# Optimization experiments

Hardware: AMD Instinct MI355X
Metric: run time of the kernel (lower is better)

## Reference

```python
import jax, jax.numpy as jnp
import numpy as np

N = 100000
E = 800000
DROPOUT_P = 0.5


def setup_inputs() -> dict:
    key = jax.random.key(0)
    ks = jax.random.split(key, 5)
    x = jax.random.normal(ks[0], (N, 128), dtype=jnp.float32)
    edge_index = jax.random.randint(ks[1], (2, E), 0, N, dtype=jnp.int32)
    # Glorot-ish init for the two GCNConv weight matrices
    W1 = jax.random.normal(ks[2], (128, 512), dtype=jnp.float32) * (1.0 / np.sqrt(128))
    b1 = jnp.zeros((512,), dtype=jnp.float32)
    W2 = jax.random.normal(ks[3], (512, 40), dtype=jnp.float32) * (1.0 / np.sqrt(512))
    b2 = jnp.zeros((40,), dtype=jnp.float32)
    return {"x": x, "edge_index": edge_index, "W1": W1, "b1": b1, "W2": W2, "b2": b2}


def _gcn_norm(edge_index, num_nodes):
    # PyG GCNConv: add self-loops, symmetric normalization D^{-1/2} (A+I) D^{-1/2}
    loop = jnp.arange(num_nodes, dtype=edge_index.dtype)
    src = jnp.concatenate([edge_index[0], loop])
    dst = jnp.concatenate([edge_index[1], loop])
    deg = jax.ops.segment_sum(jnp.ones_like(dst, dtype=jnp.float32), dst,
                              num_segments=num_nodes)
    deg_inv_sqrt = jax.lax.rsqrt(deg)  # deg >= 1 thanks to self-loops
    norm = deg_inv_sqrt[src] * deg_inv_sqrt[dst]  # [E+N]
    return src, dst, norm


def _gcn_conv(x, src, dst, norm, W, b, num_nodes):
    h = x @ W                                   # [N, out] dense GEMM first (out <= in here)
    msg = h[src] * norm[:, None]                # gather + scale: [E+N, out]
    out = jax.ops.segment_sum(msg, dst, num_segments=num_nodes)  # scatter-add
    return out + b


def reference(x, edge_index, W1, b1, W2, b2):
    src, dst, norm = _gcn_norm(edge_index, N)
    h = _gcn_conv(x, src, dst, norm, W1, b1, N)
    h = jax.nn.relu(h)
    # dropout p=0.5, training=True, deterministic mask
    keep = jax.random.bernoulli(jax.random.key(42), 1.0 - DROPOUT_P, h.shape)
    h = jnp.where(keep, h / (1.0 - DROPOUT_P), 0.0)
    hidden = h
    out = _gcn_conv(h, src, dst, norm, W2, b2, N)
    return out, hidden
```

## Files before the change

kernel.cpp:

```cpp
#include <hip/hip_runtime.h>
#include <hip/hip_bf16.h>
#include <stdint.h>

typedef __attribute__((ext_vector_type(8))) __bf16 bf16x8;
typedef __attribute__((ext_vector_type(8))) unsigned short ushort8;
typedef __attribute__((ext_vector_type(4))) float f32x4;
typedef __attribute__((ext_vector_type(4))) unsigned int u32x4;

#define N_NODES 100000
#define N_EDGES 800000
#define FIN 128
#define FH 512
#define FO 40
#define NCHUNK 391
#define TWBLKS 352

#define O_DINV   0ull
#define O_CNT    400000ull
#define O_ROWPTR 800000ull
#define O_CUR    1200016ull
#define O_SRC    1600016ull
#define O_DSRC   4800016ull
#define O_W1T    8000016ull
#define O_W2T    8131088ull
#define O_AXG    8180240ull
#define O_H2     59380240ull
#define O_PART   75380240ull
#define O_MASK   75400000ull

__device__ __forceinline__ unsigned short f2bf(float f) {
  unsigned u = __float_as_uint(f);
  u += 0x7fffu + ((u >> 16) & 1u);
  return (unsigned short)(u >> 16);
}

__device__ __forceinline__ bf16x8 pack8t(u32x4 a, u32x4 b) {
  u32x4 w;
  w.x = __builtin_amdgcn_perm(a.y, a.x, 0x07060302u);
  w.y = __builtin_amdgcn_perm(a.w, a.z, 0x07060302u);
  w.z = __builtin_amdgcn_perm(b.y, b.x, 0x07060302u);
  w.w = __builtin_amdgcn_perm(b.w, b.z, 0x07060302u);
  return __builtin_bit_cast(bf16x8, w);
}


__global__ __launch_bounds__(256) void k_count(const int* __restrict__ dst,
                                               int* __restrict__ cnt) {
  int e = blockIdx.x * 256 + threadIdx.x;
  if (e < N_EDGES) atomicAdd(&cnt[__builtin_nontemporal_load(&dst[e])], 1);
}


__global__ __launch_bounds__(256) void k_scan1tw(const int* __restrict__ cnt,
                                                 int* __restrict__ rowptr,
                                                 int* __restrict__ partials,
                                                 float* __restrict__ dinv,
                                                 const float* __restrict__ w1,
                                                 const float* __restrict__ w2,
                                                 unsigned short* __restrict__ w1t,
                                                 unsigned short* __restrict__ w2t) {
  int b = blockIdx.x;
  if (b >= NCHUNK) {
    int t = (b - NCHUNK) * 256 + threadIdx.x;
    if (t < FIN * FH) {
      int c = t >> 7, k = t & 127;
      w1t[c * 128 + k] = f2bf(w1[k * FH + c]);
    } else {
      int u = t - FIN * FH;
      int c = u >> 9, k = u & 511;
      w2t[c * FH + k] = (c < FO) ? f2bf(w2[k * FO + c]) : (unsigned short)0;
    }
    return;
  }
  int t = threadIdx.x, g = b * 256 + t;
  int v = (g < N_NODES) ? cnt[g] : 0;
  if (g < N_NODES) dinv[g] = __frsqrt_rn((float)(v + 1));
  int lane = t & 63, w = t >> 6;
  int sc = v;
#pragma unroll
  for (int off = 1; off < 64; off <<= 1) {
    int u = __shfl_up(sc, off);
    if (lane >= off) sc += u;
  }
  __shared__ int wsum[4];
  if (lane == 63) wsum[w] = sc;
  __syncthreads();
  int add = 0;
  for (int j = 0; j < w; j++) add += wsum[j];
  int incl = sc + add;
  if (g < N_NODES) rowptr[g] = incl - v;
  if (t == 255) partials[b] = incl;
}


__global__ __launch_bounds__(256) void k_scan3(int* __restrict__ rowptr,
                                               const int* __restrict__ partials,
                                               int* __restrict__ cur) {
  __shared__ int sbase;
  int t = threadIdx.x;
  int chunk = blockIdx.x;
  if (t < 64) {
    int s = 0;
    for (int j = t; j < chunk; j += 64) s += partials[j];
#pragma unroll
    for (int off = 32; off; off >>= 1) s += __shfl_down(s, off);
    if (t == 0) sbase = s;
  }
  __syncthreads();
  int base = sbase;
  int g = chunk * 256 + t;
  if (g < N_NODES) {
    int v = rowptr[g] + base;
    rowptr[g] = v;
    cur[g] = v;
  } else if (g == N_NODES) {
    rowptr[N_NODES] = N_EDGES;
  }
}

__global__ __launch_bounds__(256) void k_scatter(const int* __restrict__ src,
                                                 const int* __restrict__ dst,
                                                 const float* __restrict__ dinv,
                                                 int* __restrict__ cur,
                                                 int* __restrict__ src_sorted,
                                                 float* __restrict__ dinv_src) {
  int e = blockIdx.x * 256 + threadIdx.x;
  if (e < N_EDGES) {
    int s = __builtin_nontemporal_load(&src[e]);
    int d = __builtin_nontemporal_load(&dst[e]);
    int pos = atomicAdd(&cur[d], 1);
    src_sorted[pos] = s;
    dinv_src[pos] = dinv[s];
  }
}


__device__ __forceinline__ unsigned tf_bits(unsigned x0, unsigned x1) {
  const unsigned K0 = 0u, K1 = 42u, K2 = 0x1BD11BDAu ^ 42u;
  x0 += K0; x1 += K1;
#define RND(r) { x0 += x1; x1 = (x1 << (r)) | (x1 >> (32 - (r))); x1 ^= x0; }
  RND(13) RND(15) RND(26) RND(6)
  x0 += K1; x1 += K2 + 1u;
  RND(17) RND(29) RND(16) RND(24)
  x0 += K2; x1 += K0 + 2u;
  RND(13) RND(15) RND(26) RND(6)
  x0 += K0; x1 += K1 + 3u;
  RND(17) RND(29) RND(16) RND(24)
  x0 += K1; x1 += K2 + 4u;
  RND(13) RND(15) RND(26) RND(6)
  x0 += K2; x1 += K0 + 5u;
#undef RND
  return x0 ^ x1;
}


__global__ __launch_bounds__(256) void k_aggx(const float* __restrict__ x,
                                              const int* __restrict__ rowptr,
                                              const int* __restrict__ src_sorted,
                                              const float* __restrict__ dinv_src,
                                              const float* __restrict__ dinv,
                                              float* __restrict__ axg,
                                              unsigned char* __restrict__ mask8) {
  int i = blockIdx.x * 4 + (threadIdx.x >> 6);
  int lane = threadIdx.x & 63;
  int rs = rowptr[i], re = rowptr[i + 1];
  float di = dinv[i];
  int c = lane << 1;

  {
    unsigned fb = (unsigned)i * FH + ((unsigned)lane << 3);
    unsigned mb = 0;
#pragma unroll
    for (int q = 0; q < 8; q++)
      mb |= ((~tf_bits(0u, fb + q)) >> 31) << q;
    mask8[((size_t)i << 6) | lane] = (unsigned char)mb;
  }

  float a0 = 0.0f, a1 = 0.0f;

  for (int base = rs; base < re; base += 64) {
    int n = re - base; if (n > 64) n = 64;
    int myi = 0; float myw = 0.0f;
    if (lane < n) {
      myi = src_sorted[base + lane];
      myw = dinv_src[base + lane];
    }
    int j = 0;
    for (; j + 4 <= n; j += 4) {
      int s0 = __shfl(myi, j),     s1 = __shfl(myi, j + 1);
      int s2 = __shfl(myi, j + 2), s3 = __shfl(myi, j + 3);
      float w0 = __shfl(myw, j),      w1_ = __shfl(myw, j + 1);
      float w2_ = __shfl(myw, j + 2), w3_ = __shfl(myw, j + 3);
      float2 v0 = *(const float2*)(x + (((size_t)s0 << 7) | c));
      float2 v1 = *(const float2*)(x + (((size_t)s1 << 7) | c));
      float2 v2 = *(const float2*)(x + (((size_t)s2 << 7) | c));
      float2 v3 = *(const float2*)(x + (((size_t)s3 << 7) | c));
      a0 += w0 * v0.x + w1_ * v1.x + w2_ * v2.x + w3_ * v3.x;
      a1 += w0 * v0.y + w1_ * v1.y + w2_ * v2.y + w3_ * v3.y;
    }
    for (; j < n; j++) {
      int s0 = __shfl(myi, j);
      float w0 = __shfl(myw, j);
      float2 v0 = *(const float2*)(x + (((size_t)s0 << 7) | c));
      a0 += w0 * v0.x; a1 += w0 * v0.y;
    }
  }
  {
    float2 vs = *(const float2*)(x + (((size_t)i << 7) | c));
    a0 += di * vs.x; a1 += di * vs.y;
  }
  float2 o; o.x = a0 * di; o.y = a1 * di;
  *(float2*)(axg + (((size_t)i << 7) | c)) = o;
}


__global__ __launch_bounds__(256) void k_gemm12(const float* __restrict__ axg,
                                                const unsigned short* __restrict__ w1t,
                                                const float* __restrict__ b1,
                                                const unsigned char* __restrict__ mask8,
                                                const unsigned short* __restrict__ w2t,
                                                float* __restrict__ hidden,
                                                float* __restrict__ h2) {
  __shared__ __align__(16) char smem[32768];
  int w = threadIdx.x >> 6;
  int lane = threadIdx.x & 63;
  int m = lane & 15, kg = lane >> 4;
  int r0 = blockIdx.x * 32;
  int cw = w * 128;
  f32x4 acc[2][8];
#pragma unroll
  for (int a = 0; a < 2; a++)
#pragma unroll
    for (int t = 0; t < 8; t++)
#pragma unroll
      for (int r = 0; r < 4; r++) acc[a][t][r] = 0.0f;

  const float* xa0 = axg + (size_t)(r0 + m) * FIN + kg * 8;
  const float* xa1 = xa0 + 16 * FIN;
#pragma unroll
  for (int kc = 0; kc < 4; kc++) {
    int kb = kc * 32;
    u32x4 a0l = *(const u32x4*)(xa0 + kb);
    u32x4 a0h = *(const u32x4*)(xa0 + kb + 4);
    u32x4 a1l = *(const u32x4*)(xa1 + kb);
    u32x4 a1h = *(const u32x4*)(xa1 + kb + 4);
    bf16x8 a0 = pack8t(a0l, a0h);
    bf16x8 a1 = pack8t(a1l, a1h);
#pragma unroll
    for (int t = 0; t < 8; t++) {
      const unsigned short* bp = w1t + (size_t)(cw + t * 16 + m) * FIN + kb + kg * 8;
      bf16x8 b = __builtin_bit_cast(bf16x8, *(const ushort8*)bp);
      acc[0][t] = __builtin_amdgcn_mfma_f32_16x16x32_bf16(b, a0, acc[0][t], 0, 0, 0);
      acc[1][t] = __builtin_amdgcn_mfma_f32_16x16x32_bf16(b, a1, acc[1][t], 0, 0, 0);
    }
  }

  f32x4 bq[8];
#pragma unroll
  for (int t = 0; t < 8; t++) bq[t] = *(const f32x4*)(b1 + cw + t * 16 + kg * 4);

  u32x4 mv[2];
#pragma unroll
  for (int rt = 0; rt < 2; rt++)
    mv[rt] = *(const u32x4*)(mask8 + (size_t)(r0 + rt * 16 + m) * 64 + w * 16);

#pragma unroll
  for (int rt = 0; rt < 2; rt++) {
    int rowl = rt * 16 + m;
    int sw = (rowl & 15) << 4;
#pragma unroll
    for (int t = 0; t < 8; t++) {
      f32x4 hv;
#pragma unroll
      for (int r = 0; r < 4; r++) {
        float v = fmaxf(acc[rt][t][r] + bq[t][r], 0.0f);
        unsigned keep = (mv[rt][t >> 1] >> ((t & 1) * 16 + kg * 4 + r)) & 1u;
        hv[r] = keep ? v * 2.0f : 0.0f;
      }
      int colb = cw + t * 16 + kg * 4;
      __builtin_nontemporal_store(__builtin_bit_cast(u32x4, hv),
          (u32x4*)(hidden + (size_t)(r0 + rowl) * FH + colb));
      unsigned lo = __builtin_amdgcn_perm(__float_as_uint(hv[1]), __float_as_uint(hv[0]), 0x07060302u);
      unsigned hi = __builtin_amdgcn_perm(__float_as_uint(hv[3]), __float_as_uint(hv[2]), 0x07060302u);
      uint2 p; p.x = lo; p.y = hi;
      *(uint2*)(smem + rowl * 1024 + ((colb * 2) ^ sw)) = p;
    }
  }
  __syncthreads();

  f32x4 acc2[2][3];
#pragma unroll
  for (int rt = 0; rt < 2; rt++)
#pragma unroll
    for (int t = 0; t < 3; t++)
#pragma unroll
      for (int r = 0; r < 4; r++) acc2[rt][t][r] = 0.0f;

#pragma unroll
  for (int kc = 0; kc < 4; kc++) {
    int colk = cw + kc * 32 + kg * 8;
#pragma unroll
    for (int rt = 0; rt < 2; rt++) {
      int rowl = rt * 16 + m;
      bf16x8 a = *(const bf16x8*)(smem + rowl * 1024 + ((colk * 2) ^ ((rowl & 15) << 4)));
#pragma unroll
      for (int t = 0; t < 3; t++) {
        bf16x8 b = __builtin_bit_cast(bf16x8,
            *(const ushort8*)(w2t + (size_t)(t * 16 + m) * FH + colk));
        acc2[rt][t] = __builtin_amdgcn_mfma_f32_16x16x32_bf16(a, b, acc2[rt][t], 0, 0, 0);
      }
    }
  }
  __syncthreads();

  float* part = (float*)smem;
#pragma unroll
  for (int rt = 0; rt < 2; rt++)
#pragma unroll
    for (int t = 0; t < 3; t++)
#pragma unroll
      for (int r = 0; r < 4; r++) {
        int rowl = rt * 16 + kg * 4 + r;
        int coln = t * 16 + m;
        part[w * 1536 + rowl * 48 + coln] = acc2[rt][t][r];
      }
  __syncthreads();

  for (int idx = threadIdx.x; idx < 1536; idx += 256) {
    int rowl = idx / 48, coln = idx - rowl * 48;
    float s = part[idx] + part[1536 + idx] + part[3072 + idx] + part[4608 + idx];
    if (coln < FO) h2[(size_t)(r0 + rowl) * FO + coln] = s;
  }
}


__global__ __launch_bounds__(320) void k_agg2(const float* __restrict__ h2,
                                              const int* __restrict__ rowptr,
                                              const int* __restrict__ src_sorted,
                                              const float* __restrict__ dinv_src,
                                              const float* __restrict__ dinv,
                                              const float* __restrict__ b2,
                                              float* __restrict__ out) {
  int i = blockIdx.x * 8 + threadIdx.x / 40;
  int ch = threadIdx.x % 40;
  int rs = rowptr[i], re = rowptr[i + 1];
  float di = dinv[i];
  float acc = 0.0f;

  int e = rs;
  for (; e + 2 <= re; e += 2) {
    int s0 = src_sorted[e], s1 = src_sorted[e + 1];
    float w0 = dinv_src[e], w1_ = dinv_src[e + 1];
    float v0 = h2[(size_t)s0 * FO + ch];
    float v1 = h2[(size_t)s1 * FO + ch];
    acc += w0 * v0 + w1_ * v1;
  }
  if (e < re) {
    acc += dinv_src[e] * h2[(size_t)src_sorted[e] * FO + ch];
  }
  acc += di * h2[(size_t)i * FO + ch];
  out[(size_t)i * FO + ch] = acc * di + b2[ch];
}


extern "C" void kernel_launch(void* const* d_in, const int* in_sizes, int n_in,
                              void* d_out, int out_size, void* d_ws, size_t ws_size,
                              hipStream_t stream) {
  const float* x  = (const float*)d_in[0];
  const int* ei   = (const int*)d_in[1];
  const float* w1 = (const float*)d_in[2];
  const float* b1 = (const float*)d_in[3];
  const float* w2 = (const float*)d_in[4];
  const float* b2 = (const float*)d_in[5];

  char* ws = (char*)d_ws;
  float* dinv            = (float*)(ws + O_DINV);
  int* cnt               = (int*)(ws + O_CNT);
  int* rowptr            = (int*)(ws + O_ROWPTR);
  int* cur               = (int*)(ws + O_CUR);
  int* src_sorted        = (int*)(ws + O_SRC);
  float* dinv_src        = (float*)(ws + O_DSRC);
  unsigned short* w1t    = (unsigned short*)(ws + O_W1T);
  unsigned short* w2t    = (unsigned short*)(ws + O_W2T);
  float* axg             = (float*)(ws + O_AXG);
  float* h2              = (float*)(ws + O_H2);
  unsigned char* mask8   = (unsigned char*)(ws + O_MASK);
  int* partials          = (int*)(ws + O_PART);

  float* outp   = (float*)d_out;
  float* hidden = outp + (size_t)N_NODES * FO;

  const int* srcA = ei;
  const int* dstA = ei + N_EDGES;

  hipMemsetAsync(cnt, 0, N_NODES * sizeof(int), stream);
  k_count<<<(N_EDGES + 255) / 256, 256, 0, stream>>>(dstA, cnt);
  k_scan1tw<<<NCHUNK + TWBLKS, 256, 0, stream>>>(cnt, rowptr, partials, dinv,
                                                 w1, w2, w1t, w2t);
  k_scan3<<<NCHUNK, 256, 0, stream>>>(rowptr, partials, cur);
  k_scatter<<<(N_EDGES + 255) / 256, 256, 0, stream>>>(srcA, dstA, dinv, cur,
                                                       src_sorted, dinv_src);
  k_aggx<<<N_NODES / 4, 256, 0, stream>>>(x, rowptr, src_sorted, dinv_src, dinv,
                                          axg, mask8);
  k_gemm12<<<N_NODES / 32, 256, 0, stream>>>(axg, w1t, b1, mask8, w2t, hidden, h2);
  k_agg2<<<N_NODES / 8, 320, 0, stream>>>(h2, rowptr, src_sorted, dinv_src, dinv,
                                          b2, outp);
}
```

Before: 571.8 us.

## Fuse neighbor aggregation and dropout mask generation into the GEMM kernel

Merges the first-layer aggregation kernel into the fused GEMM kernel. Each block now aggregates its 32 rows into swizzled shared memory instead of writing a 51 MB intermediate to global memory and reading it back. The dropout mask bits are computed directly in registers rather than written to and read from a mask buffer. In exchange, each block does more serial work (8 nodes per wave in sequence), uses more shared memory, and has fewer blocks overall to hide gather latency.

After: 662.5 us. 15.9% more time.

```diff
diff --git a/kernel.cpp b/kernel.cpp
--- a/kernel.cpp
+++ b/kernel.cpp
@@ -23,10 +23,8 @@
 #define O_DSRC   4800016ull
 #define O_W1T    8000016ull
 #define O_W2T    8131088ull
-#define O_AXG    8180240ull
 #define O_H2     59380240ull
 #define O_PART   75380240ull
-#define O_MASK   75400000ull
 
 __device__ __forceinline__ unsigned short f2bf(float f) {
   unsigned u = __float_as_uint(f);
@@ -154,79 +152,85 @@
 }
 
 
-__global__ __launch_bounds__(256) void k_aggx(const float* __restrict__ x,
+__global__ __launch_bounds__(256) void k_mega(const float* __restrict__ x,
                                               const int* __restrict__ rowptr,
                                               const int* __restrict__ src_sorted,
                                               const float* __restrict__ dinv_src,
                                               const float* __restrict__ dinv,
-                                              float* __restrict__ axg,
-                                              unsigned char* __restrict__ mask8) {
-  int i = blockIdx.x * 4 + (threadIdx.x >> 6);
-  int lane = threadIdx.x & 63;
-  int rs = rowptr[i], re = rowptr[i + 1];
-  float di = dinv[i];
-  int c = lane << 1;
-
-  {
-    unsigned fb = (unsigned)i * FH + ((unsigned)lane << 3);
-    unsigned mb = 0;
-#pragma unroll
-    for (int q = 0; q < 8; q++)
-      mb |= ((~tf_bits(0u, fb + q)) >> 31) << q;
-    mask8[((size_t)i << 6) | lane] = (unsigned char)mb;
-  }
-
-  float a0 = 0.0f, a1 = 0.0f;
-
-  for (int base = rs; base < re; base += 64) {
-    int n = re - base; if (n > 64) n = 64;
-    int myi = 0; float myw = 0.0f;
-    if (lane < n) {
-      myi = src_sorted[base + lane];
-      myw = dinv_src[base + lane];
-    }
-    int j = 0;
-    for (; j + 4 <= n; j += 4) {
-      int s0 = __shfl(myi, j),     s1 = __shfl(myi, j + 1);
-      int s2 = __shfl(myi, j + 2), s3 = __shfl(myi, j + 3);
-      float w0 = __shfl(myw, j),      w1_ = __shfl(myw, j + 1);
-      float w2_ = __shfl(myw, j + 2), w3_ = __shfl(myw, j + 3);
-      float2 v0 = *(const float2*)(x + (((size_t)s0 << 7) | c));
-      float2 v1 = *(const float2*)(x + (((size_t)s1 << 7) | c));
-      float2 v2 = *(const float2*)(x + (((size_t)s2 << 7) | c));
-      float2 v3 = *(const float2*)(x + (((size_t)s3 << 7) | c));
-      a0 += w0 * v0.x + w1_ * v1.x + w2_ * v2.x + w3_ * v3.x;
-      a1 += w0 * v0.y + w1_ * v1.y + w2_ * v2.y + w3_ * v3.y;
-    }
-    for (; j < n; j++) {
-      int s0 = __shfl(myi, j);
-      float w0 = __shfl(myw, j);
-      float2 v0 = *(const float2*)(x + (((size_t)s0 << 7) | c));
-      a0 += w0 * v0.x; a1 += w0 * v0.y;
-    }
-  }
-  {
-    float2 vs = *(const float2*)(x + (((size_t)i << 7) | c));
-    a0 += di * vs.x; a1 += di * vs.y;
-  }
-  float2 o; o.x = a0 * di; o.y = a1 * di;
-  *(float2*)(axg + (((size_t)i << 7) | c)) = o;
-}
-
-
-__global__ __launch_bounds__(256) void k_gemm12(const float* __restrict__ axg,
-                                                const unsigned short* __restrict__ w1t,
-                                                const float* __restrict__ b1,
-                                                const unsigned char* __restrict__ mask8,
-                                                const unsigned short* __restrict__ w2t,
-                                                float* __restrict__ hidden,
-                                                float* __restrict__ h2) {
-  __shared__ __align__(16) char smem[32768];
+                                              const unsigned short* __restrict__ w1t,
+                                              const float* __restrict__ b1,
+                                              const unsigned short* __restrict__ w2t,
+                                              float* __restrict__ hidden,
+                                              float* __restrict__ h2) {
+  __shared__ __align__(16) char smem[49152];
   int w = threadIdx.x >> 6;
   int lane = threadIdx.x & 63;
   int m = lane & 15, kg = lane >> 4;
   int r0 = blockIdx.x * 32;
   int cw = w * 128;
+
+  unsigned km[2][4];
+#pragma unroll
+  for (int rt = 0; rt < 2; rt++) {
+    unsigned rowbase = (unsigned)(r0 + rt * 16 + m) * FH;
+#pragma unroll
+    for (int q = 0; q < 4; q++) {
+      unsigned mword = 0;
+#pragma unroll
+      for (int h = 0; h < 2; h++)
+#pragma unroll
+        for (int r = 0; r < 4; r++) {
+          unsigned col = (unsigned)(cw + (2 * q + h) * 16 + kg * 4 + r);
+          mword |= ((~tf_bits(0u, rowbase + col)) >> 31) << (h * 16 + kg * 4 + r);
+        }
+      km[rt][q] = mword;
+    }
+  }
+
+  for (int s = 0; s < 8; s++) {
+    int nl = w * 8 + s;
+    int i = r0 + nl;
+    int rs = rowptr[i], re = rowptr[i + 1];
+    float di = dinv[i];
+    int c = lane << 1;
+    float a0 = 0.0f, a1 = 0.0f;
+
+    for (int base = rs; base < re; base += 64) {
+      int n = re - base; if (n > 64) n = 64;
+      int myi = 0; float myw = 0.0f;
+      if (lane < n) {
+        myi = src_sorted[base + lane];
+        myw = dinv_src[base + lane];
+      }
+      int j = 0;
+      for (; j + 4 <= n; j += 4) {
+        int s0 = __shfl(myi, j),     s1 = __shfl(myi, j + 1);
+        int s2 = __shfl(myi, j + 2), s3 = __shfl(myi, j + 3);
+        float w0 = __shfl(myw, j),      w1_ = __shfl(myw, j + 1);
+        float w2_ = __shfl(myw, j + 2), w3_ = __shfl(myw, j + 3);
+        float2 v0 = *(const float2*)(x + (((size_t)s0 << 7) | c));
+        float2 v1 = *(const float2*)(x + (((size_t)s1 << 7) | c));
+        float2 v2 = *(const float2*)(x + (((size_t)s2 << 7) | c));
+        float2 v3 = *(const float2*)(x + (((size_t)s3 << 7) | c));
+        a0 += w0 * v0.x + w1_ * v1.x + w2_ * v2.x + w3_ * v3.x;
+        a1 += w0 * v0.y + w1_ * v1.y + w2_ * v2.y + w3_ * v3.y;
+      }
+      for (; j < n; j++) {
+        int s0 = __shfl(myi, j);
+        float w0 = __shfl(myw, j);
+        float2 v0 = *(const float2*)(x + (((size_t)s0 << 7) | c));
+        a0 += w0 * v0.x; a1 += w0 * v0.y;
+      }
+    }
+    {
+      float2 vs = *(const float2*)(x + (((size_t)i << 7) | c));
+      a0 += di * vs.x; a1 += di * vs.y;
+    }
+    float2 o; o.x = a0 * di; o.y = a1 * di;
+    *(float2*)(smem + nl * 512 + ((lane * 8) ^ ((nl & 7) << 4))) = o;
+  }
+  __syncthreads();
+
   f32x4 acc[2][8];
 #pragma unroll
   for (int a = 0; a < 2; a++)
@@ -235,15 +239,14 @@
 #pragma unroll
       for (int r = 0; r < 4; r++) acc[a][t][r] = 0.0f;
 
-  const float* xa0 = axg + (size_t)(r0 + m) * FIN + kg * 8;
-  const float* xa1 = xa0 + 16 * FIN;
 #pragma unroll
   for (int kc = 0; kc < 4; kc++) {
     int kb = kc * 32;
-    u32x4 a0l = *(const u32x4*)(xa0 + kb);
-    u32x4 a0h = *(const u32x4*)(xa0 + kb + 4);
-    u32x4 a1l = *(const u32x4*)(xa1 + kb);
-    u32x4 a1h = *(const u32x4*)(xa1 + kb + 4);
+    int cb0 = (kb + kg * 8) * 4;
+    u32x4 a0l = *(const u32x4*)(smem + m * 512 + (cb0 ^ ((m & 7) << 4)));
+    u32x4 a0h = *(const u32x4*)(smem + m * 512 + ((cb0 + 16) ^ ((m & 7) << 4)));
+    u32x4 a1l = *(const u32x4*)(smem + (16 + m) * 512 + (cb0 ^ ((m & 7) << 4)));
+    u32x4 a1h = *(const u32x4*)(smem + (16 + m) * 512 + ((cb0 + 16) ^ ((m & 7) << 4)));
     bf16x8 a0 = pack8t(a0l, a0h);
     bf16x8 a1 = pack8t(a1l, a1h);
 #pragma unroll
@@ -259,11 +262,6 @@
 #pragma unroll
   for (int t = 0; t < 8; t++) bq[t] = *(const f32x4*)(b1 + cw + t * 16 + kg * 4);
 
-  u32x4 mv[2];
-#pragma unroll
-  for (int rt = 0; rt < 2; rt++)
-    mv[rt] = *(const u32x4*)(mask8 + (size_t)(r0 + rt * 16 + m) * 64 + w * 16);
-
 #pragma unroll
   for (int rt = 0; rt < 2; rt++) {
     int rowl = rt * 16 + m;
@@ -274,7 +272,7 @@
 #pragma unroll
       for (int r = 0; r < 4; r++) {
         float v = fmaxf(acc[rt][t][r] + bq[t][r], 0.0f);
-        unsigned keep = (mv[rt][t >> 1] >> ((t & 1) * 16 + kg * 4 + r)) & 1u;
+        unsigned keep = (km[rt][t >> 1] >> ((t & 1) * 16 + kg * 4 + r)) & 1u;
         hv[r] = keep ? v * 2.0f : 0.0f;
       }
       int colb = cw + t * 16 + kg * 4;
@@ -283,7 +281,7 @@
       unsigned lo = __builtin_amdgcn_perm(__float_as_uint(hv[1]), __float_as_uint(hv[0]), 0x07060302u);
       unsigned hi = __builtin_amdgcn_perm(__float_as_uint(hv[3]), __float_as_uint(hv[2]), 0x07060302u);
       uint2 p; p.x = lo; p.y = hi;
-      *(uint2*)(smem + rowl * 1024 + ((colb * 2) ^ sw)) = p;
+      *(uint2*)(smem + 16384 + rowl * 1024 + ((colb * 2) ^ sw)) = p;
     }
   }
   __syncthreads();
@@ -302,7 +300,7 @@
 #pragma unroll
     for (int rt = 0; rt < 2; rt++) {
       int rowl = rt * 16 + m;
-      bf16x8 a = *(const bf16x8*)(smem + rowl * 1024 + ((colk * 2) ^ ((rowl & 15) << 4)));
+      bf16x8 a = *(const bf16x8*)(smem + 16384 + rowl * 1024 + ((colk * 2) ^ ((rowl & 15) << 4)));
 #pragma unroll
       for (int t = 0; t < 3; t++) {
         bf16x8 b = __builtin_bit_cast(bf16x8,
@@ -313,7 +311,7 @@
   }
   __syncthreads();
 
-  float* part = (float*)smem;
+  float* part = (float*)(smem + 16384);
 #pragma unroll
   for (int rt = 0; rt < 2; rt++)
 #pragma unroll
@@ -382,9 +380,7 @@
   float* dinv_src        = (float*)(ws + O_DSRC);
   unsigned short* w1t    = (unsigned short*)(ws + O_W1T);
   unsigned short* w2t    = (unsigned short*)(ws + O_W2T);
-  float* axg             = (float*)(ws + O_AXG);
   float* h2              = (float*)(ws + O_H2);
-  unsigned char* mask8   = (unsigned char*)(ws + O_MASK);
   int* partials          = (int*)(ws + O_PART);
 
   float* outp   = (float*)d_out;
@@ -400,9 +396,8 @@
   k_scan3<<<NCHUNK, 256, 0, stream>>>(rowptr, partials, cur);
   k_scatter<<<(N_EDGES + 255) / 256, 256, 0, stream>>>(srcA, dstA, dinv, cur,
                                                        src_sorted, dinv_src);
-  k_aggx<<<N_NODES / 4, 256, 0, stream>>>(x, rowptr, src_sorted, dinv_src, dinv,
-                                          axg, mask8);
-  k_gemm12<<<N_NODES / 32, 256, 0, stream>>>(axg, w1t, b1, mask8, w2t, hidden, h2);
+  k_mega<<<N_NODES / 32, 256, 0, stream>>>(x, rowptr, src_sorted, dinv_src, dinv,
+                                           w1t, b1, w2t, hidden, h2);
   k_agg2<<<N_NODES / 8, 320, 0, stream>>>(h2, rowptr, src_sorted, dinv_src, dinv,
                                           b2, outp);
 }
```
